# Kernel tuning notes

Measured on AMD Instinct MI355X. Metric: run time of the kernel, lower is better.

## Reference

```python
import jax, jax.numpy as jnp
import numpy as np

EPS = 1e-5

def bn_eval(x, p):
    # p: [4, C] = gamma, beta, running_mean, running_var; channel-last broadcast
    g, b, m, v = p[0], p[1], p[2], p[3]
    return (x - m) * (g / jnp.sqrt(v + EPS)) + b

def _bn_params(k, c):
    k1, k2, k3, k4 = jax.random.split(k, 4)
    gamma = jax.random.uniform(k1, (c,)) + 0.5
    beta = jax.random.normal(k2, (c,)) * 0.1
    mean = jax.random.normal(k3, (c,)) * 0.1
    var = jax.random.uniform(k4, (c,)) + 0.5
    return jnp.stack([gamma, beta, mean, var])

def _lin(k, fan_in, fan_out):
    bound = 1.0 / np.sqrt(fan_in)
    kw, kb = jax.random.split(k)
    w = jax.random.uniform(kw, (fan_in, fan_out), minval=-bound, maxval=bound)
    b = jax.random.uniform(kb, (fan_out,), minval=-bound, maxval=bound)
    return w, b

def setup_inputs() -> dict:
    key = jax.random.key(0)
    B, N, S, C, G = 2, 4096, 16, 256, 8
    ks = jax.random.split(key, 20)
    feats = jax.random.normal(ks[0], (B, N, C), dtype=jnp.float32)
    coords = jax.random.normal(ks[1], (B, N, 3), dtype=jnp.float32)
    index = jax.random.randint(ks[2], (B, N, S), 0, N, dtype=jnp.int32)
    wq, bq = _lin(ks[3], C, C); bnq = _bn_params(ks[4], C)
    wk, bk = _lin(ks[5], C, C); bnk = _bn_params(ks[6], C)
    wv, bv = _lin(ks[7], C, C)
    pm_w1, pm_b1 = _lin(ks[8], 3, C); pm_bn = _bn_params(ks[9], C)
    pm_w2, pm_b2 = _lin(ks[10], C, C)
    pb_w1, pb_b1 = _lin(ks[11], 3, C); pb_bn = _bn_params(ks[12], C)
    pb_w2, pb_b2 = _lin(ks[13], C, C)
    we_w1, we_b1 = _lin(ks[14], C, G); we_bn = _bn_params(ks[15], G)
    we_w2, we_b2 = _lin(ks[16], G, G)
    return dict(feats=feats, coords=coords, index=index,
                wq=wq, bq=bq, bnq=bnq, wk=wk, bk=bk, bnk=bnk, wv=wv, bv=bv,
                pm_w1=pm_w1, pm_b1=pm_b1, pm_bn=pm_bn, pm_w2=pm_w2, pm_b2=pm_b2,
                pb_w1=pb_w1, pb_b1=pb_b1, pb_bn=pb_bn, pb_w2=pb_w2, pb_b2=pb_b2,
                we_w1=we_w1, we_b1=we_b1, we_bn=we_bn, we_w2=we_w2, we_b2=we_b2)

def reference(feats, coords, index,
              wq, bq, bnq, wk, bk, bnk, wv, bv,
              pm_w1, pm_b1, pm_bn, pm_w2, pm_b2,
              pb_w1, pb_b1, pb_bn, pb_w2, pb_b2,
              we_w1, we_b1, we_bn, we_w2, we_b2):
    B, N, C = feats.shape
    S = index.shape[2]
    G = we_w1.shape[1]
    q = jax.nn.relu(bn_eval(feats @ wq + bq, bnq))                       # [B,N,C]
    k = jax.nn.relu(bn_eval(feats @ wk + bk, bnk))                       # [B,N,C]
    v = feats @ wv + bv                                                   # [B,N,C]
    idx = index.reshape(B, N * S)
    key_g = jnp.take_along_axis(k, idx[:, :, None], axis=1).reshape(B, N, S, C)
    val_g = jnp.take_along_axis(v, idx[:, :, None], axis=1).reshape(B, N, S, C)
    crd_g = jnp.take_along_axis(coords, idx[:, :, None], axis=1).reshape(B, N, S, 3)
    relation_qk = key_g - q[:, :, None, :]                                # [B,N,S,C]
    pos = coords[:, :, None, :] - crd_g                                   # [B,N,S,3]
    pem = jax.nn.relu(bn_eval(pos @ pm_w1 + pm_b1, pm_bn)) @ pm_w2 + pm_b2
    relation_qk = relation_qk * pem
    peb = jax.nn.relu(bn_eval(pos @ pb_w1 + pb_b1, pb_bn)) @ pb_w2 + pb_b2
    relation_qk = relation_qk + peb
    val_g = val_g + peb
    w = jax.nn.relu(bn_eval(relation_qk @ we_w1 + we_b1, we_bn)) @ we_w2 + we_b2  # [B,N,S,G]
    w = jax.nn.softmax(w, axis=2)                                         # softmax over neighbors
    val_g = val_g.reshape(B, N, S, G, C // G)
    out = jnp.einsum('bnsgi,bnsg->bngi', val_g, w).reshape(B, N, C)
    return out
```

## Files before the change

kernel.cpp:

```cpp
#include <hip/hip_runtime.h>


typedef __attribute__((ext_vector_type(8))) short bf16x8_t;
typedef __attribute__((ext_vector_type(4))) float f32x4_t;

#define BN_EPS 1e-5f
#define WSYNC() asm volatile("s_waitcnt lgkmcnt(0)" ::: "memory")

__device__ __forceinline__ float blo(unsigned int v) {
    union { unsigned int u; float f; } x; x.u = v << 16; return x.f;
}
__device__ __forceinline__ float bhi(unsigned int v) {
    union { unsigned int u; float f; } x; x.u = v & 0xffff0000u; return x.f;
}
__device__ __forceinline__ unsigned int fbits(float f) {
    union { float f; unsigned int u; } x; x.f = f; return x.u;
}
__device__ __forceinline__ unsigned short f2b(float f) {
    unsigned int u = fbits(f);
    return (unsigned short)((u + 0x7fffu + ((u >> 16) & 1u)) >> 16);
}
__device__ __forceinline__ unsigned int f2bpk(float a, float b) {
    unsigned int ua = fbits(a), ub = fbits(b);
    unsigned int ta = ua + 0x7fffu + ((ua >> 16) & 1u);
    unsigned int tb = ub + 0x7fffu + ((ub >> 16) & 1u);
    return (ta >> 16) | (tb & 0xffff0000u);
}
__device__ __forceinline__ unsigned int relpair(unsigned int kb, unsigned int qb,
                                                unsigned int pm_, unsigned int pb_) {
    float r0 = (blo(kb) - blo(qb)) * blo(pm_) + blo(pb_);
    float r1 = (bhi(kb) - bhi(qb)) * bhi(pm_) + bhi(pb_);
    return f2bpk(r0, r1);
}

__global__ __launch_bounds__(256) void k_prep(
    const float* __restrict__ wq, const float* __restrict__ wk,
    const float* __restrict__ wv, const float* __restrict__ pm2,
    const float* __restrict__ pb2,
    const float* __restrict__ pm_w1, const float* __restrict__ pm_b1,
    const float* __restrict__ pm_bn,
    const float* __restrict__ pb_w1, const float* __restrict__ pb_b1,
    const float* __restrict__ pb_bn,
    const float* __restrict__ we_w1,
    unsigned short* __restrict__ wsT, float* __restrict__ W4,
    unsigned short* __restrict__ we1TF)
{
    const int bid = blockIdx.x, t = threadIdx.x;
    if (bid < 160) {
        __shared__ unsigned short T[32][72];
        const int mat = bid >> 5;
        const int kk  = (bid >> 2) & 7;
        const int ntq = bid & 3;
        const float* s = (mat == 0) ? wq : (mat == 1) ? wk : (mat == 2) ? wv
                         : (mat == 3) ? pm2 : pb2;
        {
            int c = t & 63, r0 = t >> 6;
            for (int i = 0; i < 8; ++i) {
                int r = r0 + i * 4;
                T[r][c] = f2b(s[(kk * 32 + r) * 256 + ntq * 64 + c]);
            }
        }
        __syncthreads();
        {
            int seg = t >> 6, lane = t & 63;
            int col = seg * 16 + (lane & 15);
            int kr  = (lane >> 4) * 8;
            unsigned int v[8];
            #pragma unroll
            for (int j = 0; j < 8; ++j) v[j] = T[kr + j][col];
            uint4 o;
            o.x = v[0] | (v[1] << 16);
            o.y = v[2] | (v[3] << 16);
            o.z = v[4] | (v[5] << 16);
            o.w = v[6] | (v[7] << 16);
            *(uint4*)(wsT + mat * 65536 + (ntq * 4 + seg) * 4096 + kk * 512 + lane * 8) = o;
        }
    } else if (bid == 160) {
        int c = t;
        float s = pm_bn[c] / sqrtf(pm_bn[768 + c] + BN_EPS);
        float4 wm = make_float4(pm_w1[c] * s, pm_w1[256 + c] * s, pm_w1[512 + c] * s,
                                (pm_b1[c] - pm_bn[512 + c]) * s + pm_bn[256 + c]);
        s = pb_bn[c] / sqrtf(pb_bn[768 + c] + BN_EPS);
        float4 wb = make_float4(pb_w1[c] * s, pb_w1[256 + c] * s, pb_w1[512 + c] * s,
                                (pb_b1[c] - pb_bn[512 + c]) * s + pb_bn[256 + c]);
        ((float4*)W4)[c]       = wm;
        ((float4*)W4)[256 + c] = wb;
    } else {
        for (int j = 0; j < 8; ++j) {
            int e = t * 8 + j;
            int g = e >> 8, c = e & 255;
            we1TF[g * 256 + c] = f2b(we_w1[c * 8 + g]);
        }
    }
}

__global__ __launch_bounds__(256) void k_qkv(
    const float* __restrict__ feats,
    const unsigned short* __restrict__ wT,
    const float* __restrict__ bq, const float* __restrict__ bnq,
    const float* __restrict__ bk, const float* __restrict__ bnk,
    const float* __restrict__ bv,
    unsigned short* __restrict__ qkv)
{
    __shared__ unsigned short A[32][264];
    const int t    = threadIdx.x;
    const int widx = blockIdx.x >> 8;
    const int mb   = blockIdx.x & 255;

    for (int i = 0; i < 8; ++i) {
        int row = 4 * i + (t >> 6), col = (t & 63) * 4;
        float4 f = *(const float4*)(feats + (mb * 32 + row) * 256 + col);
        *(uint2*)&A[row][col] = make_uint2(f2bpk(f.x, f.y), f2bpk(f.z, f.w));
    }
    __syncthreads();

    const int lane = t & 63, w = t >> 6;
    const int ln15 = lane & 15, quad = lane >> 4;
    const int mt = w & 1, nh = w >> 1;

    bf16x8_t afr[8];
    #pragma unroll
    for (int kk = 0; kk < 8; ++kk)
        afr[kk] = *(const bf16x8_t*)&A[mt * 16 + ln15][kk * 32 + quad * 8];

    const unsigned short* W = wT + widx * 65536;
    const float* bias = (widx == 0) ? bq : (widx == 1) ? bk : bv;
    const float* bn   = (widx == 0) ? bnq : (widx == 1) ? bnk : nullptr;
    unsigned short* dst = qkv + (size_t)widx * 8192 * 256;

    const f32x4_t fzero = {0.f, 0.f, 0.f, 0.f};
    f32x4_t acc[8];
    for (int j = 0; j < 8; ++j) acc[j] = fzero;

    #pragma unroll
    for (int kk = 0; kk < 8; ++kk) {
        #pragma unroll
        for (int j = 0; j < 8; ++j) {
            int nt = nh * 8 + j;
            bf16x8_t bfr = *(const bf16x8_t*)(W + ((nt * 8 + kk) * 64 + lane) * 8);
            acc[j] = __builtin_amdgcn_mfma_f32_16x16x32_bf16(afr[kk], bfr, acc[j], 0, 0, 0);
        }
    }

    float bb[8], sc[8], mu[8], be[8];
    #pragma unroll
    for (int j = 0; j < 8; ++j) {
        int c = (nh * 8 + j) * 16 + ln15;
        bb[j] = bias[c];
        if (bn) {
            sc[j] = bn[c] / sqrtf(bn[768 + c] + BN_EPS);
            be[j] = bn[256 + c];
            mu[j] = bn[512 + c];
        }
    }
    __syncthreads();
    #pragma unroll
    for (int j = 0; j < 8; ++j) {
        int c = (nh * 8 + j) * 16 + ln15;
        float y[4];
        for (int r = 0; r < 4; ++r) {
            y[r] = acc[j][r] + bb[j];
            if (bn) y[r] = fmaxf((y[r] - mu[j]) * sc[j] + be[j], 0.f);
        }
        for (int r = 0; r < 4; r += 2) {
            unsigned int pk = f2bpk(y[r], y[r + 1]);
            A[mt * 16 + quad * 4 + r][c]     = (unsigned short)pk;
            A[mt * 16 + quad * 4 + r + 1][c] = (unsigned short)(pk >> 16);
        }
    }
    __syncthreads();
    {
        int row = t >> 3, cc = (t & 7) * 32;
        #pragma unroll
        for (int j = 0; j < 4; ++j) {
            uint4 v = *(const uint4*)&A[row][cc + 8 * j];
            *(uint4*)(dst + (mb * 32 + row) * 256 + cc + 8 * j) = v;
        }
    }
}

__global__ __launch_bounds__(256, 2) void k_main(
    const float* __restrict__ coords,
    const int*   __restrict__ index,
    const unsigned short* __restrict__ qm,
    const unsigned short* __restrict__ km,
    const unsigned short* __restrict__ vm,
    const unsigned short* __restrict__ pmw2F,
    const unsigned short* __restrict__ pbw2F,
    const float* __restrict__ W4,
    const unsigned short* __restrict__ we1TF,
    const float* __restrict__ pm_b2, const float* __restrict__ pb_b2,
    const float* __restrict__ we_b1, const float* __restrict__ we_bn,
    const float* __restrict__ we_w2, const float* __restrict__ we_b2,
    float* __restrict__ out)
{
    __shared__ unsigned short bufR[64][264];
    __shared__ unsigned short bufP[64][264];
    __shared__ float posA[64][4];
    __shared__ float us_[64][8];
    __shared__ int   rowg_[64];
    __shared__ float we2s[8][8];
    __shared__ float web2[8];

    const int t  = threadIdx.x;
    const int P0 = blockIdx.x * 4;
    const int bb_ = P0 >> 12;
    const int w = t >> 6, lane = t & 63;
    const int ln15 = lane & 15, quad = lane >> 4;
    const int R0 = w * 16;
    const int Pg = P0 + w;

    const int rg = (bb_ << 12) + index[Pg * 16 + ln15];
    uint4 kpre[8];
    #pragma unroll
    for (int kk = 0; kk < 8; ++kk)
        kpre[kk] = *(const uint4*)(km + rg * 256 + kk * 32 + quad * 8);

    const int hc = lane * 4;
    float4 cm[4], cb[4];
    #pragma unroll
    for (int i = 0; i < 4; ++i) {
        cm[i] = ((const float4*)W4)[hc + i];
        cb[i] = ((const float4*)W4)[256 + hc + i];
    }

    const int g8 = ln15 & 7;
    const float swe_r = we_bn[g8] / sqrtf(we_bn[24 + g8] + BN_EPS);
    const float dwe_r = (we_b1[g8] - we_bn[16 + g8]) * swe_r + we_bn[8 + g8];

    if (lane < 16) {
        rowg_[R0 + lane] = rg;
        posA[R0 + lane][0] = coords[Pg * 3 + 0] - coords[rg * 3 + 0];
        posA[R0 + lane][1] = coords[Pg * 3 + 1] - coords[rg * 3 + 1];
        posA[R0 + lane][2] = coords[Pg * 3 + 2] - coords[rg * 3 + 2];
        posA[R0 + lane][3] = 0.f;
    }
    if (t < 64) we2s[t >> 3][t & 7] = we_w2[t];
    if (t < 8)  web2[t] = we_b2[t];
    WSYNC();

    const f32x4_t fzero = {0.f, 0.f, 0.f, 0.f};

    #pragma unroll
    for (int m = 0; m < 16; ++m) {
        float4 p = *(const float4*)&posA[R0 + m][0];
        float h0 = fmaxf(p.x * cb[0].x + p.y * cb[0].y + p.z * cb[0].z + cb[0].w, 0.f);
        float h1 = fmaxf(p.x * cb[1].x + p.y * cb[1].y + p.z * cb[1].z + cb[1].w, 0.f);
        float h2 = fmaxf(p.x * cb[2].x + p.y * cb[2].y + p.z * cb[2].z + cb[2].w, 0.f);
        float h3 = fmaxf(p.x * cb[3].x + p.y * cb[3].y + p.z * cb[3].z + cb[3].w, 0.f);
        *(uint2*)&bufR[R0 + m][hc] = make_uint2(f2bpk(h0, h1), f2bpk(h2, h3));
    }
    __syncthreads();

    f32x4_t acc[4][4];
    for (int a = 0; a < 4; ++a) for (int mt = 0; mt < 4; ++mt) acc[a][mt] = fzero;
    #pragma unroll
    for (int kk = 0; kk < 8; ++kk) {
        bf16x8_t afr[4];
        #pragma unroll
        for (int mt = 0; mt < 4; ++mt)
            afr[mt] = *(const bf16x8_t*)&bufR[mt * 16 + ln15][kk * 32 + quad * 8];
        #pragma unroll
        for (int ntl = 0; ntl < 4; ++ntl) {
            int nt = w * 4 + ntl;
            bf16x8_t bfr = *(const bf16x8_t*)(pbw2F + ((nt * 8 + kk) * 64 + lane) * 8);
            #pragma unroll
            for (int mt = 0; mt < 4; ++mt)
                acc[ntl][mt] = __builtin_amdgcn_mfma_f32_16x16x32_bf16(afr[mt], bfr, acc[ntl][mt], 0, 0, 0);
        }
    }
    __syncthreads();

    #pragma unroll
    for (int ntl = 0; ntl < 4; ++ntl) {
        int c = (w * 4 + ntl) * 16 + ln15;
        float bbv = pb_b2[c];
        for (int mt = 0; mt < 4; ++mt)
            for (int r = 0; r < 4; r += 2) {
                unsigned int pk = f2bpk(acc[ntl][mt][r] + bbv, acc[ntl][mt][r + 1] + bbv);
                bufP[mt * 16 + quad * 4 + r][c]     = (unsigned short)pk;
                bufP[mt * 16 + quad * 4 + r + 1][c] = (unsigned short)(pk >> 16);
            }
    }
    #pragma unroll
    for (int m = 0; m < 16; ++m) {
        float4 p = *(const float4*)&posA[R0 + m][0];
        float h0 = fmaxf(p.x * cm[0].x + p.y * cm[0].y + p.z * cm[0].z + cm[0].w, 0.f);
        float h1 = fmaxf(p.x * cm[1].x + p.y * cm[1].y + p.z * cm[1].z + cm[1].w, 0.f);
        float h2 = fmaxf(p.x * cm[2].x + p.y * cm[2].y + p.z * cm[2].z + cm[2].w, 0.f);
        float h3 = fmaxf(p.x * cm[3].x + p.y * cm[3].y + p.z * cm[3].z + cm[3].w, 0.f);
        *(uint2*)&bufR[R0 + m][hc] = make_uint2(f2bpk(h0, h1), f2bpk(h2, h3));
    }
    __syncthreads();

    for (int a = 0; a < 4; ++a) for (int mt = 0; mt < 4; ++mt) acc[a][mt] = fzero;
    #pragma unroll
    for (int kk = 0; kk < 8; ++kk) {
        bf16x8_t afr[4];
        #pragma unroll
        for (int mt = 0; mt < 4; ++mt)
            afr[mt] = *(const bf16x8_t*)&bufR[mt * 16 + ln15][kk * 32 + quad * 8];
        #pragma unroll
        for (int ntl = 0; ntl < 4; ++ntl) {
            int nt = w * 4 + ntl;
            bf16x8_t bfr = *(const bf16x8_t*)(pmw2F + ((nt * 8 + kk) * 64 + lane) * 8);
            #pragma unroll
            for (int mt = 0; mt < 4; ++mt)
                acc[ntl][mt] = __builtin_amdgcn_mfma_f32_16x16x32_bf16(afr[mt], bfr, acc[ntl][mt], 0, 0, 0);
        }
    }
    __syncthreads();

    #pragma unroll
    for (int ntl = 0; ntl < 4; ++ntl) {
        int c = (w * 4 + ntl) * 16 + ln15;
        float bbv = pm_b2[c];
        for (int mt = 0; mt < 4; ++mt)
            for (int r = 0; r < 4; r += 2) {
                unsigned int pk = f2bpk(acc[ntl][mt][r] + bbv, acc[ntl][mt][r + 1] + bbv);
                bufR[mt * 16 + quad * 4 + r][c]     = (unsigned short)pk;
                bufR[mt * 16 + quad * 4 + r + 1][c] = (unsigned short)(pk >> 16);
            }
    }
    __syncthreads();

    {
        const bf16x8_t bz = {0, 0, 0, 0, 0, 0, 0, 0};
        f32x4_t lacc = fzero;
        #pragma unroll
        for (int kk = 0; kk < 8; ++kk) {
            int cb8 = kk * 32 + quad * 8;
            uint4 pm4 = *(const uint4*)&bufR[R0 + ln15][cb8];
            uint4 pb4 = *(const uint4*)&bufP[R0 + ln15][cb8];
            uint4 q4  = *(const uint4*)(qm + Pg * 256 + cb8);
            union { uint4 u; bf16x8_t v; } rr;
            rr.u.x = relpair(kpre[kk].x, q4.x, pm4.x, pb4.x);
            rr.u.y = relpair(kpre[kk].y, q4.y, pm4.y, pb4.y);
            rr.u.z = relpair(kpre[kk].z, q4.z, pm4.z, pb4.z);
            rr.u.w = relpair(kpre[kk].w, q4.w, pm4.w, pb4.w);
            bf16x8_t bfr = bz;
            if (ln15 < 8) bfr = *(const bf16x8_t*)(we1TF + ln15 * 256 + cb8);
            lacc = __builtin_amdgcn_mfma_f32_16x16x32_bf16(rr.v, bfr, lacc, 0, 0, 0);
        }
        if (ln15 < 8) {
            #pragma unroll
            for (int r = 0; r < 4; ++r)
                us_[R0 + quad * 4 + r][ln15] = fmaxf(lacc[r] * swe_r + dwe_r, 0.f);
        }
    }
    WSYNC();

    if (lane < 16) {
        float uv[8], l[8];
        #pragma unroll
        for (int gp = 0; gp < 8; ++gp) uv[gp] = us_[R0 + lane][gp];
        #pragma unroll
        for (int g = 0; g < 8; ++g) {
            float x = web2[g];
            for (int gp = 0; gp < 8; ++gp) x += uv[gp] * we2s[gp][g];
            l[g] = x;
        }
        #pragma unroll
        for (int g = 0; g < 8; ++g) us_[R0 + lane][g] = l[g];
    }
    WSYNC();

    if (lane < 8) {
        int g = lane;
        float mx = -1e30f;
        for (int s = 0; s < 16; ++s) mx = fmaxf(mx, us_[R0 + s][g]);
        float e[16], sum = 0.f;
        for (int s = 0; s < 16; ++s) { e[s] = __expf(us_[R0 + s][g] - mx); sum += e[s]; }
        float inv = 1.f / sum;
        for (int s = 0; s < 16; ++s) us_[R0 + s][g] = e[s] * inv;
    }
    WSYNC();

    {
        int c5 = lane * 4, g = lane >> 3;
        float a0 = 0.f, a1 = 0.f, a2 = 0.f, a3 = 0.f;
        #pragma unroll
        for (int s = 0; s < 16; ++s) {
            int rv = rowg_[R0 + s];
            float wv_ = us_[R0 + s][g];
            uint2 v4 = *(const uint2*)(vm + rv * 256 + c5);
            uint2 p4 = *(const uint2*)&bufP[R0 + s][c5];
            a0 += wv_ * (blo(v4.x) + blo(p4.x));
            a1 += wv_ * (bhi(v4.x) + bhi(p4.x));
            a2 += wv_ * (blo(v4.y) + blo(p4.y));
            a3 += wv_ * (bhi(v4.y) + bhi(p4.y));
        }
        *(float4*)(out + (size_t)Pg * 256 + c5) = make_float4(a0, a1, a2, a3);
    }
}

extern "C" void kernel_launch(void* const* d_in, const int* in_sizes, int n_in,
                              void* d_out, int out_size, void* d_ws, size_t ws_size,
                              hipStream_t stream)
{
    const float* feats  = (const float*)d_in[0];
    const float* coords = (const float*)d_in[1];
    const int*   index  = (const int*)d_in[2];
    const float* wq     = (const float*)d_in[3];
    const float* bq     = (const float*)d_in[4];
    const float* bnq    = (const float*)d_in[5];
    const float* wk     = (const float*)d_in[6];
    const float* bk     = (const float*)d_in[7];
    const float* bnk    = (const float*)d_in[8];
    const float* wv     = (const float*)d_in[9];
    const float* bv     = (const float*)d_in[10];
    const float* pm_w1  = (const float*)d_in[11];
    const float* pm_b1  = (const float*)d_in[12];
    const float* pm_bn  = (const float*)d_in[13];
    const float* pm_w2  = (const float*)d_in[14];
    const float* pm_b2  = (const float*)d_in[15];
    const float* pb_w1  = (const float*)d_in[16];
    const float* pb_b1  = (const float*)d_in[17];
    const float* pb_bn  = (const float*)d_in[18];
    const float* pb_w2  = (const float*)d_in[19];
    const float* pb_b2  = (const float*)d_in[20];
    const float* we_w1  = (const float*)d_in[21];
    const float* we_b1  = (const float*)d_in[22];
    const float* we_bn  = (const float*)d_in[23];
    const float* we_w2  = (const float*)d_in[24];
    const float* we_b2  = (const float*)d_in[25];

    unsigned short* qkv   = (unsigned short*)d_ws;
    unsigned short* wsT   = qkv + (size_t)3 * 8192 * 256;
    float*          W4    = (float*)(wsT + 5 * 65536);
    unsigned short* we1TF = (unsigned short*)(W4 + 2048);

    const size_t need = (size_t)13238272 + 8192 + 4096;
    if (ws_size < need) {
        hipMemsetAsync(d_out, 0, (size_t)out_size * 4, stream);
        return;
    }

    k_prep<<<162,  256, 0, stream>>>(wq, wk, wv, pm_w2, pb_w2,
                                     pm_w1, pm_b1, pm_bn,
                                     pb_w1, pb_b1, pb_bn,
                                     we_w1, wsT, W4, we1TF);
    k_qkv <<<768,  256, 0, stream>>>(feats, wsT, bq, bnq, bk, bnk, bv, qkv);
    k_main<<<2048, 256, 0, stream>>>(coords, index,
                                     qkv,
                                     qkv + (size_t)8192 * 256,
                                     qkv + (size_t)2 * 8192 * 256,
                                     wsT + 3 * 65536,
                                     wsT + 4 * 65536,
                                     W4, we1TF,
                                     pm_b2, pb_b2,
                                     we_b1, we_bn, we_w2, we_b2,
                                     (float*)d_out);
}
```

Before: 206.1 us.

## Fuse weight prep into QKV kernel and prefetch q/v gathers in main kernel

The separate weight-prep launch is merged into the QKV GEMM kernel. QKV blocks now convert fp32 weights to bf16 directly into shared memory and load feats straight into registers, using 64-row by 128-column tiles. The main kernel prefetches q rows and gathered v rows into registers up front, folds the positional biases into the accumulator initialisation, and switches to the library bf16 pack intrinsic. This removes one launch and one serial dependency, and hides the gather latency. In exchange it uses more registers and redoes the weight conversion in every QKV block.

New measurement: 239.4 us. +16.2%, slower.

```diff
diff --git a/kernel.cpp b/kernel.cpp
--- a/kernel.cpp
+++ b/kernel.cpp
@@ -1,4 +1,5 @@
 #include <hip/hip_runtime.h>
+#include <hip/hip_bf16.h>
 
 
 typedef __attribute__((ext_vector_type(8))) short bf16x8_t;
@@ -21,10 +22,9 @@
     return (unsigned short)((u + 0x7fffu + ((u >> 16) & 1u)) >> 16);
 }
 __device__ __forceinline__ unsigned int f2bpk(float a, float b) {
-    unsigned int ua = fbits(a), ub = fbits(b);
-    unsigned int ta = ua + 0x7fffu + ((ua >> 16) & 1u);
-    unsigned int tb = ub + 0x7fffu + ((ub >> 16) & 1u);
-    return (ta >> 16) | (tb & 0xffff0000u);
+    union { __hip_bfloat162 h; unsigned int u; } x;
+    x.h = __float22bfloat162_rn(make_float2(a, b));
+    return x.u;
 }
 __device__ __forceinline__ unsigned int relpair(unsigned int kb, unsigned int qb,
                                                 unsigned int pm_, unsigned int pb_) {
@@ -33,149 +33,167 @@
     return f2bpk(r0, r1);
 }
 
-__global__ __launch_bounds__(256) void k_prep(
-    const float* __restrict__ wq, const float* __restrict__ wk,
-    const float* __restrict__ wv, const float* __restrict__ pm2,
-    const float* __restrict__ pb2,
-    const float* __restrict__ pm_w1, const float* __restrict__ pm_b1,
-    const float* __restrict__ pm_bn,
-    const float* __restrict__ pb_w1, const float* __restrict__ pb_b1,
-    const float* __restrict__ pb_bn,
-    const float* __restrict__ we_w1,
-    unsigned short* __restrict__ wsT, float* __restrict__ W4,
-    unsigned short* __restrict__ we1TF)
-{
-    const int bid = blockIdx.x, t = threadIdx.x;
-    if (bid < 160) {
-        __shared__ unsigned short T[32][72];
-        const int mat = bid >> 5;
-        const int kk  = (bid >> 2) & 7;
-        const int ntq = bid & 3;
-        const float* s = (mat == 0) ? wq : (mat == 1) ? wk : (mat == 2) ? wv
-                         : (mat == 3) ? pm2 : pb2;
-        {
-            int c = t & 63, r0 = t >> 6;
-            for (int i = 0; i < 8; ++i) {
-                int r = r0 + i * 4;
-                T[r][c] = f2b(s[(kk * 32 + r) * 256 + ntq * 64 + c]);
-            }
-        }
-        __syncthreads();
-        {
-            int seg = t >> 6, lane = t & 63;
-            int col = seg * 16 + (lane & 15);
-            int kr  = (lane >> 4) * 8;
-            unsigned int v[8];
-            #pragma unroll
-            for (int j = 0; j < 8; ++j) v[j] = T[kr + j][col];
-            uint4 o;
-            o.x = v[0] | (v[1] << 16);
-            o.y = v[2] | (v[3] << 16);
-            o.z = v[4] | (v[5] << 16);
-            o.w = v[6] | (v[7] << 16);
-            *(uint4*)(wsT + mat * 65536 + (ntq * 4 + seg) * 4096 + kk * 512 + lane * 8) = o;
-        }
-    } else if (bid == 160) {
-        int c = t;
-        float s = pm_bn[c] / sqrtf(pm_bn[768 + c] + BN_EPS);
-        float4 wm = make_float4(pm_w1[c] * s, pm_w1[256 + c] * s, pm_w1[512 + c] * s,
-                                (pm_b1[c] - pm_bn[512 + c]) * s + pm_bn[256 + c]);
-        s = pb_bn[c] / sqrtf(pb_bn[768 + c] + BN_EPS);
-        float4 wb = make_float4(pb_w1[c] * s, pb_w1[256 + c] * s, pb_w1[512 + c] * s,
-                                (pb_b1[c] - pb_bn[512 + c]) * s + pb_bn[256 + c]);
-        ((float4*)W4)[c]       = wm;
-        ((float4*)W4)[256 + c] = wb;
-    } else {
-        for (int j = 0; j < 8; ++j) {
-            int e = t * 8 + j;
-            int g = e >> 8, c = e & 255;
-            we1TF[g * 256 + c] = f2b(we_w1[c * 8 + g]);
-        }
-    }
-}
-
 __global__ __launch_bounds__(256) void k_qkv(
     const float* __restrict__ feats,
-    const unsigned short* __restrict__ wT,
-    const float* __restrict__ bq, const float* __restrict__ bnq,
-    const float* __restrict__ bk, const float* __restrict__ bnk,
-    const float* __restrict__ bv,
-    unsigned short* __restrict__ qkv)
+    const float* __restrict__ wq, const float* __restrict__ bq, const float* __restrict__ bnq,
+    const float* __restrict__ wk, const float* __restrict__ bk, const float* __restrict__ bnk,
+    const float* __restrict__ wv, const float* __restrict__ bv,
+    const float* __restrict__ pm2, const float* __restrict__ pb2,
+    const float* __restrict__ pm_w1, const float* __restrict__ pm_b1, const float* __restrict__ pm_bn,
+    const float* __restrict__ pb_w1, const float* __restrict__ pb_b1, const float* __restrict__ pb_bn,
+    const float* __restrict__ we_w1,
+    unsigned short* __restrict__ qkv, unsigned short* __restrict__ wsT,
+    float* __restrict__ W4, unsigned short* __restrict__ we1TF)
 {
-    __shared__ unsigned short A[32][264];
-    const int t    = threadIdx.x;
-    const int widx = blockIdx.x >> 8;
-    const int mb   = blockIdx.x & 255;
-
-    for (int i = 0; i < 8; ++i) {
-        int row = 4 * i + (t >> 6), col = (t & 63) * 4;
-        float4 f = *(const float4*)(feats + (mb * 32 + row) * 256 + col);
-        *(uint2*)&A[row][col] = make_uint2(f2bpk(f.x, f.y), f2bpk(f.z, f.w));
-    }
-    __syncthreads();
-
-    const int lane = t & 63, w = t >> 6;
-    const int ln15 = lane & 15, quad = lane >> 4;
-    const int mt = w & 1, nh = w >> 1;
-
-    bf16x8_t afr[8];
-    #pragma unroll
-    for (int kk = 0; kk < 8; ++kk)
-        afr[kk] = *(const bf16x8_t*)&A[mt * 16 + ln15][kk * 32 + quad * 8];
-
-    const unsigned short* W = wT + widx * 65536;
+    __shared__ __align__(16) unsigned short LSH[128 * 264];
+    const int bid = blockIdx.x, t = threadIdx.x;
+
+    if (bid >= 768) {
+        if (bid < 832) {
+            unsigned short (*T)[72] = (unsigned short(*)[72])LSH;
+            int bp  = bid - 768;
+            int mat = 3 + (bp >> 5);
+            int sub = bp & 31;
+            int kk  = sub >> 2, ntq = sub & 3;
+            const float* s = (mat == 3) ? pm2 : pb2;
+            {
+                int c = t & 63, r0 = t >> 6;
+                for (int i = 0; i < 8; ++i) {
+                    int r = r0 + i * 4;
+                    T[r][c] = f2b(s[(kk * 32 + r) * 256 + ntq * 64 + c]);
+                }
+            }
+            __syncthreads();
+            {
+                int seg = t >> 6, lane = t & 63;
+                int col = seg * 16 + (lane & 15);
+                int kr  = (lane >> 4) * 8;
+                unsigned int v[8];
+                #pragma unroll
+                for (int j = 0; j < 8; ++j) v[j] = T[kr + j][col];
+                uint4 o;
+                o.x = v[0] | (v[1] << 16);
+                o.y = v[2] | (v[3] << 16);
+                o.z = v[4] | (v[5] << 16);
+                o.w = v[6] | (v[7] << 16);
+                *(uint4*)(wsT + mat * 65536 + (ntq * 4 + seg) * 4096 + kk * 512 + lane * 8) = o;
+            }
+        } else if (bid == 832) {
+            int c = t;
+            float s = pm_bn[c] / sqrtf(pm_bn[768 + c] + BN_EPS);
+            float4 wm = make_float4(pm_w1[c] * s, pm_w1[256 + c] * s, pm_w1[512 + c] * s,
+                                    (pm_b1[c] - pm_bn[512 + c]) * s + pm_bn[256 + c]);
+            s = pb_bn[c] / sqrtf(pb_bn[768 + c] + BN_EPS);
+            float4 wb = make_float4(pb_w1[c] * s, pb_w1[256 + c] * s, pb_w1[512 + c] * s,
+                                    (pb_b1[c] - pb_bn[512 + c]) * s + pb_bn[256 + c]);
+            ((float4*)W4)[c]       = wm;
+            ((float4*)W4)[256 + c] = wb;
+        } else {
+            for (int j = 0; j < 8; ++j) {
+                int e = t * 8 + j;
+                int g = e >> 8, c = e & 255;
+                we1TF[g * 256 + c] = f2b(we_w1[c * 8 + g]);
+            }
+        }
+        return;
+    }
+
+    const int widx = bid >> 8;
+    const int rem  = bid & 255;
+    const int nh   = rem & 1;
+    const int mb   = rem >> 1;
+
+    const float* W    = (widx == 0) ? wq : (widx == 1) ? wk : wv;
     const float* bias = (widx == 0) ? bq : (widx == 1) ? bk : bv;
     const float* bn   = (widx == 0) ? bnq : (widx == 1) ? bnk : nullptr;
     unsigned short* dst = qkv + (size_t)widx * 8192 * 256;
 
-    const f32x4_t fzero = {0.f, 0.f, 0.f, 0.f};
+    const int lane = t & 63, w = t >> 6;
+    const int ln15 = lane & 15, quad = lane >> 4;
+
+    bf16x8_t afr[8];
+    {
+        int row = mb * 64 + w * 16 + ln15;
+        #pragma unroll
+        for (int kk = 0; kk < 8; ++kk) {
+            const float* p = feats + row * 256 + kk * 32 + quad * 8;
+            float4 fa = *(const float4*)p;
+            float4 fb = *(const float4*)(p + 4);
+            union { unsigned int u[4]; bf16x8_t v; } x;
+            x.u[0] = f2bpk(fa.x, fa.y);
+            x.u[1] = f2bpk(fa.z, fa.w);
+            x.u[2] = f2bpk(fb.x, fb.y);
+            x.u[3] = f2bpk(fb.z, fb.w);
+            afr[kk] = x.v;
+        }
+    }
+    float scv[8], ddv[8];
+    #pragma unroll
+    for (int j = 0; j < 8; ++j) {
+        int c = nh * 128 + j * 16 + ln15;
+        float bb = bias[c];
+        if (bn) {
+            float s = bn[c] / sqrtf(bn[768 + c] + BN_EPS);
+            scv[j] = s;
+            ddv[j] = (bb - bn[512 + c]) * s + bn[256 + c];
+        } else { scv[j] = 1.f; ddv[j] = bb; }
+    }
+
+    {
+        const int nloc = t & 127, kq = t >> 7;
+        const float* Wb = W + nh * 128 + nloc;
+        for (int it = 0; it < 32; ++it) {
+            int k0 = it * 8 + kq * 4;
+            float w0 = Wb[(k0    ) * 256];
+            float w1 = Wb[(k0 + 1) * 256];
+            float w2 = Wb[(k0 + 2) * 256];
+            float w3 = Wb[(k0 + 3) * 256];
+            *(uint2*)&LSH[nloc * 264 + k0] = make_uint2(f2bpk(w0, w1), f2bpk(w2, w3));
+        }
+    }
+    __syncthreads();
+
     f32x4_t acc[8];
-    for (int j = 0; j < 8; ++j) acc[j] = fzero;
-
+    #pragma unroll
+    for (int j = 0; j < 8; ++j) acc[j] = (f32x4_t){0.f, 0.f, 0.f, 0.f};
     #pragma unroll
     for (int kk = 0; kk < 8; ++kk) {
         #pragma unroll
         for (int j = 0; j < 8; ++j) {
-            int nt = nh * 8 + j;
-            bf16x8_t bfr = *(const bf16x8_t*)(W + ((nt * 8 + kk) * 64 + lane) * 8);
+            bf16x8_t bfr = *(const bf16x8_t*)&LSH[(j * 16 + ln15) * 264 + kk * 32 + quad * 8];
             acc[j] = __builtin_amdgcn_mfma_f32_16x16x32_bf16(afr[kk], bfr, acc[j], 0, 0, 0);
         }
     }
-
-    float bb[8], sc[8], mu[8], be[8];
+    __syncthreads();
+
+    unsigned short (*Ct)[136] = (unsigned short(*)[136])LSH;
     #pragma unroll
     for (int j = 0; j < 8; ++j) {
-        int c = (nh * 8 + j) * 16 + ln15;
-        bb[j] = bias[c];
-        if (bn) {
-            sc[j] = bn[c] / sqrtf(bn[768 + c] + BN_EPS);
-            be[j] = bn[256 + c];
-            mu[j] = bn[512 + c];
-        }
-    }
-    __syncthreads();
-    #pragma unroll
-    for (int j = 0; j < 8; ++j) {
-        int c = (nh * 8 + j) * 16 + ln15;
         float y[4];
+        #pragma unroll
         for (int r = 0; r < 4; ++r) {
-            y[r] = acc[j][r] + bb[j];
-            if (bn) y[r] = fmaxf((y[r] - mu[j]) * sc[j] + be[j], 0.f);
-        }
+            y[r] = acc[j][r] * scv[j] + ddv[j];
+            if (bn) y[r] = fmaxf(y[r], 0.f);
+        }
+        int cl = j * 16 + ln15;
         for (int r = 0; r < 4; r += 2) {
             unsigned int pk = f2bpk(y[r], y[r + 1]);
-            A[mt * 16 + quad * 4 + r][c]     = (unsigned short)pk;
-            A[mt * 16 + quad * 4 + r + 1][c] = (unsigned short)(pk >> 16);
+            Ct[w * 16 + quad * 4 + r][cl]     = (unsigned short)pk;
+            Ct[w * 16 + quad * 4 + r + 1][cl] = (unsigned short)(pk >> 16);
         }
     }
     __syncthreads();
     {
-        int row = t >> 3, cc = (t & 7) * 32;
-        #pragma unroll
-        for (int j = 0; j < 4; ++j) {
-            uint4 v = *(const uint4*)&A[row][cc + 8 * j];
-            *(uint4*)(dst + (mb * 32 + row) * 256 + cc + 8 * j) = v;
-        }
+        int row = t >> 2, c0 = (t & 3) * 32;
+        uint4 v0 = *(const uint4*)&Ct[row][c0];
+        uint4 v1 = *(const uint4*)&Ct[row][c0 + 8];
+        uint4 v2 = *(const uint4*)&Ct[row][c0 + 16];
+        uint4 v3 = *(const uint4*)&Ct[row][c0 + 24];
+        unsigned short* d = dst + (mb * 64 + row) * 256 + nh * 128 + c0;
+        *(uint4*)(d)      = v0;
+        *(uint4*)(d + 8)  = v1;
+        *(uint4*)(d + 16) = v2;
+        *(uint4*)(d + 24) = v3;
     }
 }
 
@@ -198,7 +216,6 @@
     __shared__ unsigned short bufP[64][264];
     __shared__ float posA[64][4];
     __shared__ float us_[64][8];
-    __shared__ int   rowg_[64];
     __shared__ float we2s[8][8];
     __shared__ float web2[8];
 
@@ -211,11 +228,25 @@
     const int Pg = P0 + w;
 
     const int rg = (bb_ << 12) + index[Pg * 16 + ln15];
-    uint4 kpre[8];
-    #pragma unroll
-    for (int kk = 0; kk < 8; ++kk)
+    uint4 kpre[8], qpre[8];
+    #pragma unroll
+    for (int kk = 0; kk < 8; ++kk) {
         kpre[kk] = *(const uint4*)(km + rg * 256 + kk * 32 + quad * 8);
-
+        qpre[kk] = *(const uint4*)(qm + Pg * 256 + kk * 32 + quad * 8);
+    }
+    uint2 vpre[16];
+    #pragma unroll
+    for (int s = 0; s < 16; ++s) {
+        int rv = (bb_ << 12) + index[Pg * 16 + s];
+        vpre[s] = *(const uint2*)(vm + rv * 256 + lane * 4);
+    }
+    float bb0[4], bb1[4];
+    #pragma unroll
+    for (int ntl = 0; ntl < 4; ++ntl) {
+        int c = (w * 4 + ntl) * 16 + ln15;
+        bb0[ntl] = pb_b2[c];
+        bb1[ntl] = pm_b2[c];
+    }
     const int hc = lane * 4;
     float4 cm[4], cb[4];
     #pragma unroll
@@ -223,23 +254,20 @@
         cm[i] = ((const float4*)W4)[hc + i];
         cb[i] = ((const float4*)W4)[256 + hc + i];
     }
-
     const int g8 = ln15 & 7;
     const float swe_r = we_bn[g8] / sqrtf(we_bn[24 + g8] + BN_EPS);
     const float dwe_r = (we_b1[g8] - we_bn[16 + g8]) * swe_r + we_bn[8 + g8];
 
     if (lane < 16) {
-        rowg_[R0 + lane] = rg;
-        posA[R0 + lane][0] = coords[Pg * 3 + 0] - coords[rg * 3 + 0];
-        posA[R0 + lane][1] = coords[Pg * 3 + 1] - coords[rg * 3 + 1];
-        posA[R0 + lane][2] = coords[Pg * 3 + 2] - coords[rg * 3 + 2];
+        int rgs = (bb_ << 12) + index[Pg * 16 + lane];
+        posA[R0 + lane][0] = coords[Pg * 3 + 0] - coords[rgs * 3 + 0];
+        posA[R0 + lane][1] = coords[Pg * 3 + 1] - coords[rgs * 3 + 1];
+        posA[R0 + lane][2] = coords[Pg * 3 + 2] - coords[rgs * 3 + 2];
         posA[R0 + lane][3] = 0.f;
     }
     if (t < 64) we2s[t >> 3][t & 7] = we_w2[t];
     if (t < 8)  web2[t] = we_b2[t];
     WSYNC();
-
-    const f32x4_t fzero = {0.f, 0.f, 0.f, 0.f};
 
     #pragma unroll
     for (int m = 0; m < 16; ++m) {
@@ -253,7 +281,10 @@
     __syncthreads();
 
     f32x4_t acc[4][4];
-    for (int a = 0; a < 4; ++a) for (int mt = 0; mt < 4; ++mt) acc[a][mt] = fzero;
+    #pragma unroll
+    for (int a = 0; a < 4; ++a)
+        for (int mt = 0; mt < 4; ++mt)
+            acc[a][mt] = (f32x4_t){bb0[a], bb0[a], bb0[a], bb0[a]};
     #pragma unroll
     for (int kk = 0; kk < 8; ++kk) {
         bf16x8_t afr[4];
@@ -274,10 +305,9 @@
     #pragma unroll
     for (int ntl = 0; ntl < 4; ++ntl) {
         int c = (w * 4 + ntl) * 16 + ln15;
-        float bbv = pb_b2[c];
         for (int mt = 0; mt < 4; ++mt)
             for (int r = 0; r < 4; r += 2) {
-                unsigned int pk = f2bpk(acc[ntl][mt][r] + bbv, acc[ntl][mt][r + 1] + bbv);
+                unsigned int pk = f2bpk(acc[ntl][mt][r], acc[ntl][mt][r + 1]);
                 bufP[mt * 16 + quad * 4 + r][c]     = (unsigned short)pk;
                 bufP[mt * 16 + quad * 4 + r + 1][c] = (unsigned short)(pk >> 16);
             }
@@ -293,7 +323,10 @@
     }
     __syncthreads();
 
-    for (int a = 0; a < 4; ++a) for (int mt = 0; mt < 4; ++mt) acc[a][mt] = fzero;
+    #pragma unroll
+    for (int a = 0; a < 4; ++a)
+        for (int mt = 0; mt < 4; ++mt)
+            acc[a][mt] = (f32x4_t){bb1[a], bb1[a], bb1[a], bb1[a]};
     #pragma unroll
     for (int kk = 0; kk < 8; ++kk) {
         bf16x8_t afr[4];
@@ -314,10 +347,9 @@
     #pragma unroll
     for (int ntl = 0; ntl < 4; ++ntl) {
         int c = (w * 4 + ntl) * 16 + ln15;
-        float bbv = pm_b2[c];
         for (int mt = 0; mt < 4; ++mt)
             for (int r = 0; r < 4; r += 2) {
-                unsigned int pk = f2bpk(acc[ntl][mt][r] + bbv, acc[ntl][mt][r + 1] + bbv);
+                unsigned int pk = f2bpk(acc[ntl][mt][r], acc[ntl][mt][r + 1]);
                 bufR[mt * 16 + quad * 4 + r][c]     = (unsigned short)pk;
                 bufR[mt * 16 + quad * 4 + r + 1][c] = (unsigned short)(pk >> 16);
             }
@@ -326,18 +358,17 @@
 
     {
         const bf16x8_t bz = {0, 0, 0, 0, 0, 0, 0, 0};
-        f32x4_t lacc = fzero;
+        f32x4_t lacc = {0.f, 0.f, 0.f, 0.f};
         #pragma unroll
         for (int kk = 0; kk < 8; ++kk) {
             int cb8 = kk * 32 + quad * 8;
             uint4 pm4 = *(const uint4*)&bufR[R0 + ln15][cb8];
             uint4 pb4 = *(const uint4*)&bufP[R0 + ln15][cb8];
-            uint4 q4  = *(const uint4*)(qm + Pg * 256 + cb8);
             union { uint4 u; bf16x8_t v; } rr;
-            rr.u.x = relpair(kpre[kk].x, q4.x, pm4.x, pb4.x);
-            rr.u.y = relpair(kpre[kk].y, q4.y, pm4.y, pb4.y);
-            rr.u.z = relpair(kpre[kk].z, q4.z, pm4.z, pb4.z);
-            rr.u.w = relpair(kpre[kk].w, q4.w, pm4.w, pb4.w);
+            rr.u.x = relpair(kpre[kk].x, qpre[kk].x, pm4.x, pb4.x);
+            rr.u.y = relpair(kpre[kk].y, qpre[kk].y, pm4.y, pb4.y);
+            rr.u.z = relpair(kpre[kk].z, qpre[kk].z, pm4.z, pb4.z);
+            rr.u.w = relpair(kpre[kk].w, qpre[kk].w, pm4.w, pb4.w);
             bf16x8_t bfr = bz;
             if (ln15 < 8) bfr = *(const bf16x8_t*)(we1TF + ln15 * 256 + cb8);
             lacc = __builtin_amdgcn_mfma_f32_16x16x32_bf16(rr.v, bfr, lacc, 0, 0, 0);
@@ -381,9 +412,8 @@
         float a0 = 0.f, a1 = 0.f, a2 = 0.f, a3 = 0.f;
         #pragma unroll
         for (int s = 0; s < 16; ++s) {
-            int rv = rowg_[R0 + s];
             float wv_ = us_[R0 + s][g];
-            uint2 v4 = *(const uint2*)(vm + rv * 256 + c5);
+            uint2 v4 = vpre[s];
             uint2 p4 = *(const uint2*)&bufP[R0 + s][c5];
             a0 += wv_ * (blo(v4.x) + blo(p4.x));
             a1 += wv_ * (bhi(v4.x) + bhi(p4.x));
@@ -436,11 +466,13 @@
         return;
     }
 
-    k_prep<<<162,  256, 0, stream>>>(wq, wk, wv, pm_w2, pb_w2,
+    k_qkv <<<834,  256, 0, stream>>>(feats,
+                                     wq, bq, bnq, wk, bk, bnk, wv, bv,
+                                     pm_w2, pb_w2,
                                      pm_w1, pm_b1, pm_bn,
                                      pb_w1, pb_b1, pb_bn,
-                                     we_w1, wsT, W4, we1TF);
-    k_qkv <<<768,  256, 0, stream>>>(feats, wsT, bq, bnq, bk, bnk, bv, qkv);
+                                     we_w1,
+                                     qkv, wsT, W4, we1TF);
     k_main<<<2048, 256, 0, stream>>>(coords, index,
                                      qkv,
                                      qkv + (size_t)8192 * 256,
```
